# Performance work log

Hardware: AMD Instinct MI355X
Metric: run time of the kernel (lower is better)

## Reference

```python
import jax, jax.numpy as jnp
import numpy as np

N_NODES = 70000
N_EDGES = 2_000_000
IN_CH, FEAT_CH, OUT_CH = 1044, 128, 3


def _gcn_norm(src_sl, dst_sl, n_nodes, dtype):
    # PyG gcn_norm with add_self_loops=True, edge_weight=1:
    # deg over target nodes, norm = deg^-1/2[src] * deg^-1/2[dst]
    deg = jax.ops.segment_sum(jnp.ones(src_sl.shape[0], dtype=dtype), dst_sl,
                              num_segments=n_nodes)
    dinv = jnp.where(deg > 0, jax.lax.rsqrt(deg), jnp.zeros((), dtype))
    return dinv[src_sl] * dinv[dst_sl]


def _gcn_layer(x, src_sl, dst_sl, norm, W, b, n_nodes):
    h = x @ W                                  # [N, out] linear transform first
    msg = h[src_sl] * norm[:, None]            # gather + scale
    out = jax.ops.segment_sum(msg, dst_sl, num_segments=n_nodes)  # scatter-add
    return out + b


def setup_inputs() -> dict:
    key = jax.random.key(0)
    ks = jax.random.split(key, 6)
    features = jax.random.normal(ks[0], (N_NODES, IN_CH), dtype=jnp.float32)
    edges = jax.random.randint(ks[1], (2, N_EDGES), 0, N_NODES, dtype=jnp.int64)
    edges2 = jax.random.randint(ks[2], (2, N_EDGES), 0, N_NODES, dtype=jnp.int64)
    edge_features = jax.random.normal(ks[3], (N_EDGES,), dtype=jnp.float32)
    W1 = jax.random.normal(ks[4], (IN_CH, FEAT_CH), dtype=jnp.float32) * (1.0 / np.sqrt(IN_CH))
    b1 = jnp.zeros((FEAT_CH,), dtype=jnp.float32)
    W2 = jax.random.normal(ks[5], (FEAT_CH, OUT_CH), dtype=jnp.float32) * (1.0 / np.sqrt(FEAT_CH))
    b2 = jnp.zeros((OUT_CH,), dtype=jnp.float32)
    return {"features": features, "edges": edges, "edges2": edges2,
            "edge_features": edge_features, "W1": W1, "b1": b1, "W2": W2, "b2": b2}


def reference(features, edges, edges2, edge_features, W1, b1, W2, b2):
    # edge_features is discarded by the module (set to None); edges2 unused.
    n = features.shape[0]
    loop = jnp.arange(n, dtype=edges.dtype)
    src_sl = jnp.concatenate([edges[0], loop])  # self-loops appended
    dst_sl = jnp.concatenate([edges[1], loop])
    norm = _gcn_norm(src_sl, dst_sl, n, features.dtype)
    x = _gcn_layer(features, src_sl, dst_sl, norm, W1, b1, n)
    x = jax.nn.relu(x)
    # dropout is identity in eval mode (deterministic reference)
    return _gcn_layer(x, src_sl, dst_sl, norm, W2, b2, n)
```

## Files before the change

### kernel.cpp

```cpp
#include <hip/hip_runtime.h>
#include <hip/hip_bf16.h>

#define K_IN   1044
#define N_FEAT 128
#define KPAD2  1088
#define NST2   17
#define BM     96

#define NB     512
#define BWMAX  256
#define EPB    8192

typedef __attribute__((ext_vector_type(8))) short short8;
typedef __attribute__((ext_vector_type(4))) float f32x4;

__device__ __forceinline__ ushort f2bf(float f) {
  unsigned x = __float_as_uint(f);
  x += 0x7fffu + ((x >> 16) & 1u);
  return (ushort)(x >> 16);
}
__device__ __forceinline__ uint pkbf(float lo, float hi) {
  __hip_bfloat162 h = __float22bfloat162_rn(make_float2(lo, hi));
  return *reinterpret_cast<uint*>(&h);
}
__device__ __forceinline__ float bflo(uint v) { return __uint_as_float(v << 16); }
__device__ __forceinline__ float bfhi(uint v) { return __uint_as_float(v & 0xFFFF0000u); }

__device__ __forceinline__ void gld16(const void* g, void* l) {
  __builtin_amdgcn_global_load_lds(
      (const __attribute__((address_space(1))) unsigned int*)g,
      (__attribute__((address_space(3))) unsigned int*)l, 16, 0, 0);
}


__global__ __launch_bounds__(256) void convw1_hist_kernel(const float* __restrict__ W1,
                                                          ushort* __restrict__ W1T,
                                                          const int* __restrict__ dst,
                                                          int* __restrict__ bt,
                                                          int E, int bw, int convBlocks) {
  if ((int)blockIdx.x < convBlocks) {
    int idx = blockIdx.x * 256 + threadIdx.x;
    if (idx >= N_FEAT * KPAD2) return;
    int col = idx / KPAD2, k = idx - col * KPAD2;
    int kk = k & ~63;
    int jp = (k >> 3) & 7;
    int e  = k & 7;
    int jl = jp ^ (col & 7);
    int ksrc = kk + 8 * jl + e;
    W1T[idx] = (ksrc < K_IN) ? f2bf(W1[(size_t)ksrc * N_FEAT + col]) : (ushort)0;
  } else {
    __shared__ int h[NB];
    const int t = threadIdx.x;
    for (int i = t; i < NB; i += 256) h[i] = 0;
    __syncthreads();
    const int e0 = (blockIdx.x - convBlocks) * EPB;
    const int e1 = min(e0 + EPB, E);
    for (int e = e0 + t; e < e1; e += 256) atomicAdd(&h[dst[e] / bw], 1);
    __syncthreads();
    for (int i = t; i < NB; i += 256)
      if (h[i]) atomicAdd(&bt[i], h[i]);
  }
}

__global__ __launch_bounds__(256) void csr_bucket_scan_kernel(const int* __restrict__ bt,
                                                              int* __restrict__ bucket_base,
                                                              int* __restrict__ bucket_cursor) {
  __shared__ int sc[256];
  const int t = threadIdx.x;
  int v0 = bt[2 * t], v1 = bt[2 * t + 1];
  int s = v0 + v1;
  sc[t] = s;
  __syncthreads();
  for (int off = 1; off < 256; off <<= 1) {
    int x = (t >= off) ? sc[t - off] : 0;
    __syncthreads();
    sc[t] += x;
    __syncthreads();
  }
  int excl = sc[t] - s;
  bucket_base[2 * t]     = excl;
  bucket_base[2 * t + 1] = excl + v0;
  bucket_cursor[2 * t]     = excl;
  bucket_cursor[2 * t + 1] = excl + v0;
  if (t == 255) bucket_base[NB] = sc[255];
}

__global__ __launch_bounds__(256) void csr_stage_kernel(const int* __restrict__ src,
                                                        const int* __restrict__ dst,
                                                        int* __restrict__ bucket_cursor,
                                                        uint* __restrict__ staging, int E, int bw) {
  __shared__ int h[NB];
  __shared__ int cur[NB];
  const int t = threadIdx.x;
  for (int i = t; i < NB; i += 256) h[i] = 0;
  __syncthreads();
  const int e0 = blockIdx.x * EPB;
  const int e1 = min(e0 + EPB, E);
  for (int e = e0 + t; e < e1; e += 256) atomicAdd(&h[dst[e] / bw], 1);
  __syncthreads();
  for (int i = t; i < NB; i += 256)
    cur[i] = h[i] ? atomicAdd(&bucket_cursor[i], h[i]) : 0;
  __syncthreads();
  for (int e = e0 + t; e < e1; e += 256) {
    int d = dst[e];
    int b = d / bw;
    int p = atomicAdd(&cur[b], 1);
    staging[p] = ((uint)src[e] << 8) | (uint)(d - b * bw);
  }
}

__global__ __launch_bounds__(256) void csr_final_kernel(const uint* __restrict__ staging,
                                                        const int* __restrict__ bucket_base,
                                                        int* __restrict__ row_ptr,
                                                        int* __restrict__ sorted_src,
                                                        float* __restrict__ dinv,
                                                        int N, int bw, int E) {
  __shared__ int hist[BWMAX];
  __shared__ int sc[256];
  const int b = blockIdx.x;
  const int t = threadIdx.x;
  if (b == 0 && t == 0) row_ptr[N] = E;
  const int node0 = b * bw;
  const int nn = min(bw, N - node0);
  if (nn <= 0) return;
  const int base = bucket_base[b];
  const int cnt  = bucket_base[b + 1] - base;

  for (int i = t; i < BWMAX; i += 256) hist[i] = 0;
  __syncthreads();
  for (int i = t; i < cnt; i += 256)
    atomicAdd(&hist[staging[base + i] & 255u], 1);
  __syncthreads();
  int v = (t < nn) ? hist[t] : 0;
  if (t < nn) dinv[node0 + t] = rsqrtf((float)(v + 1));
  sc[t] = v;
  __syncthreads();
  for (int off = 1; off < 256; off <<= 1) {
    int x = (t >= off) ? sc[t - off] : 0;
    __syncthreads();
    sc[t] += x;
    __syncthreads();
  }
  int excl = sc[t] - v;
  if (t < nn) row_ptr[node0 + t] = base + excl;
  if (t < nn) hist[t] = excl;
  __syncthreads();
  for (int i = t; i < cnt; i += 256) {
    uint p = staging[base + i];
    int c = atomicAdd(&hist[p & 255u], 1);
    sorted_src[base + c] = (int)(p >> 8);
  }
}


__global__ __launch_bounds__(256) void gemm1_mfma_kernel(const float* __restrict__ X,
                                                         const ushort* __restrict__ W1T,
                                                         const float* __restrict__ dinv,
                                                         ushort* __restrict__ G1, int M) {
  __shared__ float  Af[2][BM * 64];
  __shared__ ushort Bsb[2][128 * 64];

  const int t = threadIdx.x;
  const int row0 = blockIdx.x * BM;
  const int w = t >> 6, l = t & 63;
  const int w24 = w * 24, w32 = w * 32;
  const int Mm1 = M - 1;

  const int wm = w >> 1, wn = w & 1;
  const int lr = l & 15, g = l >> 4;

  f32x4 acc[3][4] = {};

  auto stage = [&](int s, int buf) {
    const int kk = s * 64;
    #pragma unroll
    for (int i = 0; i < 6; i++) {
      int r  = w24 + 4 * i + (l >> 4);
      int jl = (l & 15) ^ (r & 15);
      int grow = min(row0 + r, Mm1);
      int gk   = min(kk + 4 * jl, K_IN - 4);
      gld16(X + (size_t)grow * K_IN + gk, (void*)&Af[buf][(w24 + 4 * i) * 64]);
    }
    #pragma unroll
    for (int i = 0; i < 4; i++) {
      int c = w32 + 8 * i + (l >> 3);
      gld16(W1T + (size_t)c * KPAD2 + kk + 8 * (l & 7),
            (void*)&Bsb[buf][(w32 + 8 * i) * 64]);
    }
  };

  stage(0, 0);
  __syncthreads();

  int cur = 0;
  #pragma unroll 1
  for (int s = 0; s < NST2; s++) {
    if (s + 1 < NST2) stage(s + 1, cur ^ 1);

    #pragma unroll
    for (int ss = 0; ss < 2; ss++) {
      short8 af[3], bfr[4];
      #pragma unroll
      for (int m = 0; m < 3; m++) {
        const int row = wm * 48 + m * 16 + lr;
        const float* rp = &Af[cur][row * 64];
        const int c0 = (ss * 8 + 2 * g)     ^ (row & 15);
        const int c1 = (ss * 8 + 2 * g + 1) ^ (row & 15);
        float4 a0 = *(const float4*)&rp[c0 * 4];
        float4 a1 = *(const float4*)&rp[c1 * 4];
        uint4 uu = make_uint4(pkbf(a0.x, a0.y), pkbf(a0.z, a0.w),
                              pkbf(a1.x, a1.y), pkbf(a1.z, a1.w));
        af[m] = *(short8*)&uu;
      }
      #pragma unroll
      for (int n = 0; n < 4; n++) {
        const int col = wn * 64 + n * 16 + lr;
        const int cB = (ss * 4 + g) ^ (col & 7);
        bfr[n] = *(const short8*)&Bsb[cur][col * 64 + cB * 8];
      }
      #pragma unroll
      for (int m = 0; m < 3; m++)
        #pragma unroll
        for (int n = 0; n < 4; n++)
          acc[m][n] = __builtin_amdgcn_mfma_f32_16x16x32_bf16(af[m], bfr[n], acc[m][n], 0, 0, 0);
    }

    __syncthreads();
    cur ^= 1;
  }

  const int rbase = row0 + wm * 48 + g * 4;
  const int cbase = wn * 64 + lr;
  #pragma unroll
  for (int m = 0; m < 3; m++) {
    #pragma unroll
    for (int r = 0; r < 4; r++) {
      int row = rbase + m * 16 + r;
      if (row < M) {
        float dv = dinv[row];
        #pragma unroll
        for (int n = 0; n < 4; n++)
          G1[(size_t)row * N_FEAT + cbase + n * 16] = f2bf(dv * acc[m][n][r]);
      }
    }
  }
}


__global__ __launch_bounds__(256) void agg1mm_kernel(const ushort* __restrict__ G1,
                                                     const int* __restrict__ row_ptr,
                                                     const int* __restrict__ sorted_src,
                                                     const float* __restrict__ dinv,
                                                     const float* __restrict__ b1,
                                                     const float* __restrict__ W2,
                                                     float* __restrict__ G2, int N) {
  const int w = (blockIdx.x * blockDim.x + threadIdx.x) >> 6;
  const int lane = threadIdx.x & 63;
  if (w >= N) return;
  const int beg = row_ptr[w], end = row_ptr[w + 1];
  const uint* g1u = (const uint*)G1;
  const int co = lane;

  uint vs = g1u[((size_t)w << 6) + co];
  float a0 = bflo(vs), a1 = bfhi(vs);

  int e = beg;
  for (; e + 16 <= end; e += 16) {
    int s[16];
    #pragma unroll
    for (int i = 0; i < 16; i++) s[i] = sorted_src[e + i];
    uint v[16];
    #pragma unroll
    for (int i = 0; i < 16; i++) v[i] = g1u[((size_t)s[i] << 6) + co];
    #pragma unroll
    for (int i = 0; i < 16; i++) { a0 += bflo(v[i]); a1 += bfhi(v[i]); }
  }
  for (; e + 4 <= end; e += 4) {
    int s[4];
    #pragma unroll
    for (int i = 0; i < 4; i++) s[i] = sorted_src[e + i];
    uint v[4];
    #pragma unroll
    for (int i = 0; i < 4; i++) v[i] = g1u[((size_t)s[i] << 6) + co];
    #pragma unroll
    for (int i = 0; i < 4; i++) { a0 += bflo(v[i]); a1 += bfhi(v[i]); }
  }
  for (; e < end; e++) {
    uint v = g1u[((size_t)sorted_src[e] << 6) + co];
    a0 += bflo(v); a1 += bfhi(v);
  }

  const float di = dinv[w];
  float r0 = fmaxf(fmaf(di, a0, b1[2 * co + 0]), 0.f);
  float r1 = fmaxf(fmaf(di, a1, b1[2 * co + 1]), 0.f);

  const float* wrow = W2 + 6 * co;
  float s0 = r0 * wrow[0] + r1 * wrow[3];
  float s1 = r0 * wrow[1] + r1 * wrow[4];
  float s2 = r0 * wrow[2] + r1 * wrow[5];
  #pragma unroll
  for (int off = 32; off > 0; off >>= 1) {
    s0 += __shfl_down(s0, off);
    s1 += __shfl_down(s1, off);
    s2 += __shfl_down(s2, off);
  }
  if (lane == 0) {
    *(float4*)&G2[(size_t)w * 4] = make_float4(di * s0, di * s1, di * s2, 0.f);
  }
}


__global__ __launch_bounds__(256) void agg2_kernel(const float* __restrict__ G2,
                                                   const int* __restrict__ row_ptr,
                                                   const int* __restrict__ sorted_src,
                                                   const float* __restrict__ dinv,
                                                   const float* __restrict__ b2,
                                                   float* __restrict__ out, int N) {
  int t = blockIdx.x * blockDim.x + threadIdx.x;
  int node = t >> 6, lane = t & 63;
  if (node >= N) return;
  int beg = row_ptr[node], end = row_ptr[node + 1];
  float a0 = 0.f, a1 = 0.f, a2 = 0.f;
  for (int e = beg + lane; e < end; e += 64) {
    float4 v = *(const float4*)&G2[(size_t)sorted_src[e] * 4];
    a0 += v.x; a1 += v.y; a2 += v.z;
  }
  #pragma unroll
  for (int off = 32; off > 0; off >>= 1) {
    a0 += __shfl_down(a0, off);
    a1 += __shfl_down(a1, off);
    a2 += __shfl_down(a2, off);
  }
  if (lane == 0) {
    float di = dinv[node];
    float4 self = *(const float4*)&G2[(size_t)node * 4];
    out[node * 3 + 0] = di * (a0 + self.x) + b2[0];
    out[node * 3 + 1] = di * (a1 + self.y) + b2[1];
    out[node * 3 + 2] = di * (a2 + self.z) + b2[2];
  }
}


extern "C" void kernel_launch(void* const* d_in, const int* in_sizes, int n_in,
                              void* d_out, int out_size, void* d_ws, size_t ws_size,
                              hipStream_t stream) {
  const float* features = (const float*)d_in[0];
  const int*   edges    = (const int*)d_in[1];
  const float* W1 = (const float*)d_in[4];
  const float* b1 = (const float*)d_in[5];
  const float* W2 = (const float*)d_in[6];
  const float* b2 = (const float*)d_in[7];
  float* out = (float*)d_out;

  const int N = in_sizes[0] / K_IN;
  const int E = in_sizes[1] / 2;
  const int* src = edges;
  const int* dst = edges + E;
  const int bw = (N + NB - 1) / NB;

  char* ws = (char*)d_ws;
  size_t off = 0;
  auto alloc = [&](size_t bytes) {
    void* p = ws + off;
    off += (bytes + 255) & ~(size_t)255;
    return p;
  };
  int*    bt            = (int*)   alloc((size_t)NB * sizeof(int));
  int*    bucket_base   = (int*)   alloc((size_t)(NB + 1) * sizeof(int));
  int*    bucket_cursor = (int*)   alloc((size_t)NB * sizeof(int));
  int*    row_ptr       = (int*)   alloc((size_t)(N + 1) * sizeof(int));
  float*  dinv          = (float*) alloc((size_t)N * sizeof(float));
  uint*   staging       = (uint*)  alloc((size_t)E * sizeof(uint));
  int*    sorted_src    = (int*)   alloc((size_t)E * sizeof(int));
  ushort* G1            = (ushort*)alloc((size_t)N * N_FEAT * sizeof(ushort));
  float*  G2            = (float*) alloc((size_t)N * 4 * sizeof(float));
  ushort* W1T           = (ushort*)alloc((size_t)N_FEAT * KPAD2 * sizeof(ushort));
  (void)ws_size;

  const int eblocks = (E + EPB - 1) / EPB;
  const int convBlocks = (N_FEAT * KPAD2 + 255) / 256;

  hipMemsetAsync(bt, 0, (size_t)NB * sizeof(int), stream);
  convw1_hist_kernel<<<convBlocks + eblocks, 256, 0, stream>>>(W1, W1T, dst, bt, E, bw, convBlocks);
  csr_bucket_scan_kernel<<<1, 256, 0, stream>>>(bt, bucket_base, bucket_cursor);
  csr_stage_kernel<<<eblocks, 256, 0, stream>>>(src, dst, bucket_cursor, staging, E, bw);
  csr_final_kernel<<<NB, 256, 0, stream>>>(staging, bucket_base, row_ptr, sorted_src, dinv, N, bw, E);
  gemm1_mfma_kernel<<<(N + BM - 1) / BM, 256, 0, stream>>>(features, W1T, dinv, G1, N);
  agg1mm_kernel<<<((size_t)N * 64 + 255) / 256, 256, 0, stream>>>(G1, row_ptr, sorted_src, dinv, b1, W2, G2, N);
  agg2_kernel<<<((size_t)N * 64 + 255) / 256, 256, 0, stream>>>(G2, row_ptr, sorted_src, dinv, b2, out, N);
}
```

Measured before the change: 248.7 us.

## Use per-block bucket counts with global scan; halve agg2 threads per node

The histogram kernel now writes per-block, per-bucket counts to a bucket-major matrix instead of atomically accumulating global bucket totals. A single-block scan turns that matrix into exclusive offsets and bucket bases. The stage kernel then reads its precomputed offsets directly, which removes its second histogram pass, the global atomics and the memset. Separately, agg2 assigns 32 lanes per node instead of 64 to suit the low average degree, at the cost of a serial single-block scan over about 125K entries.

```diff
diff --git a/kernel.cpp b/kernel.cpp
--- a/kernel.cpp
+++ b/kernel.cpp
@@ -36,8 +36,9 @@
 __global__ __launch_bounds__(256) void convw1_hist_kernel(const float* __restrict__ W1,
                                                           ushort* __restrict__ W1T,
                                                           const int* __restrict__ dst,
-                                                          int* __restrict__ bt,
-                                                          int E, int bw, int convBlocks) {
+                                                          int* __restrict__ pbc,
+                                                          int E, int bw, int convBlocks,
+                                                          int eblocks) {
   if ((int)blockIdx.x < convBlocks) {
     int idx = blockIdx.x * 256 + threadIdx.x;
     if (idx >= N_FEAT * KPAD2) return;
@@ -51,56 +52,57 @@
   } else {
     __shared__ int h[NB];
     const int t = threadIdx.x;
+    const int blk = blockIdx.x - convBlocks;
     for (int i = t; i < NB; i += 256) h[i] = 0;
     __syncthreads();
-    const int e0 = (blockIdx.x - convBlocks) * EPB;
+    const int e0 = blk * EPB;
     const int e1 = min(e0 + EPB, E);
     for (int e = e0 + t; e < e1; e += 256) atomicAdd(&h[dst[e] / bw], 1);
     __syncthreads();
-    for (int i = t; i < NB; i += 256)
-      if (h[i]) atomicAdd(&bt[i], h[i]);
-  }
-}
-
-__global__ __launch_bounds__(256) void csr_bucket_scan_kernel(const int* __restrict__ bt,
-                                                              int* __restrict__ bucket_base,
-                                                              int* __restrict__ bucket_cursor) {
-  __shared__ int sc[256];
+    for (int i = t; i < NB; i += 256) pbc[i * eblocks + blk] = h[i];
+  }
+}
+
+__global__ __launch_bounds__(256) void csr_scan2_kernel(int* __restrict__ pbc,
+                                                        int* __restrict__ bucket_base,
+                                                        int eblocks, int total, int E) {
+  __shared__ int sums[256];
   const int t = threadIdx.x;
-  int v0 = bt[2 * t], v1 = bt[2 * t + 1];
-  int s = v0 + v1;
-  sc[t] = s;
+  const int chunk = (total + 255) / 256;
+  const int beg = t * chunk;
+  const int end = min(beg + chunk, total);
+  int s = 0;
+  for (int i = beg; i < end; i++) s += pbc[i];
+  sums[t] = s;
   __syncthreads();
   for (int off = 1; off < 256; off <<= 1) {
-    int x = (t >= off) ? sc[t - off] : 0;
-    __syncthreads();
-    sc[t] += x;
-    __syncthreads();
-  }
-  int excl = sc[t] - s;
-  bucket_base[2 * t]     = excl;
-  bucket_base[2 * t + 1] = excl + v0;
-  bucket_cursor[2 * t]     = excl;
-  bucket_cursor[2 * t + 1] = excl + v0;
-  if (t == 255) bucket_base[NB] = sc[255];
+    int x = (t >= off) ? sums[t - off] : 0;
+    __syncthreads();
+    sums[t] += x;
+    __syncthreads();
+  }
+  int run = sums[t] - s;
+  for (int i = beg; i < end; i++) {
+    int v = pbc[i];
+    pbc[i] = run;
+    if (i % eblocks == 0) bucket_base[i / eblocks] = run;
+    run += v;
+  }
+  if (t == 255) bucket_base[NB] = E;
 }
 
 __global__ __launch_bounds__(256) void csr_stage_kernel(const int* __restrict__ src,
                                                         const int* __restrict__ dst,
-                                                        int* __restrict__ bucket_cursor,
-                                                        uint* __restrict__ staging, int E, int bw) {
-  __shared__ int h[NB];
+                                                        const int* __restrict__ pbc,
+                                                        uint* __restrict__ staging, int E, int bw,
+                                                        int eblocks) {
   __shared__ int cur[NB];
   const int t = threadIdx.x;
-  for (int i = t; i < NB; i += 256) h[i] = 0;
-  __syncthreads();
-  const int e0 = blockIdx.x * EPB;
+  const int blk = blockIdx.x;
+  for (int i = t; i < NB; i += 256) cur[i] = pbc[i * eblocks + blk];
+  __syncthreads();
+  const int e0 = blk * EPB;
   const int e1 = min(e0 + EPB, E);
-  for (int e = e0 + t; e < e1; e += 256) atomicAdd(&h[dst[e] / bw], 1);
-  __syncthreads();
-  for (int i = t; i < NB; i += 256)
-    cur[i] = h[i] ? atomicAdd(&bucket_cursor[i], h[i]) : 0;
-  __syncthreads();
   for (int e = e0 + t; e < e1; e += 256) {
     int d = dst[e];
     int b = d / bw;
@@ -317,19 +319,19 @@
                                                    const float* __restrict__ b2,
                                                    float* __restrict__ out, int N) {
   int t = blockIdx.x * blockDim.x + threadIdx.x;
-  int node = t >> 6, lane = t & 63;
+  int node = t >> 5, lane = t & 31;
   if (node >= N) return;
   int beg = row_ptr[node], end = row_ptr[node + 1];
   float a0 = 0.f, a1 = 0.f, a2 = 0.f;
-  for (int e = beg + lane; e < end; e += 64) {
+  for (int e = beg + lane; e < end; e += 32) {
     float4 v = *(const float4*)&G2[(size_t)sorted_src[e] * 4];
     a0 += v.x; a1 += v.y; a2 += v.z;
   }
   #pragma unroll
-  for (int off = 32; off > 0; off >>= 1) {
-    a0 += __shfl_down(a0, off);
-    a1 += __shfl_down(a1, off);
-    a2 += __shfl_down(a2, off);
+  for (int off = 16; off > 0; off >>= 1) {
+    a0 += __shfl_down(a0, off, 32);
+    a1 += __shfl_down(a1, off, 32);
+    a2 += __shfl_down(a2, off, 32);
   }
   if (lane == 0) {
     float di = dinv[node];
@@ -365,9 +367,10 @@
     off += (bytes + 255) & ~(size_t)255;
     return p;
   };
-  int*    bt            = (int*)   alloc((size_t)NB * sizeof(int));
+  const int eblocks = (E + EPB - 1) / EPB;
+
+  int*    pbc           = (int*)   alloc((size_t)NB * eblocks * sizeof(int));
   int*    bucket_base   = (int*)   alloc((size_t)(NB + 1) * sizeof(int));
-  int*    bucket_cursor = (int*)   alloc((size_t)NB * sizeof(int));
   int*    row_ptr       = (int*)   alloc((size_t)(N + 1) * sizeof(int));
   float*  dinv          = (float*) alloc((size_t)N * sizeof(float));
   uint*   staging       = (uint*)  alloc((size_t)E * sizeof(uint));
@@ -377,15 +380,13 @@
   ushort* W1T           = (ushort*)alloc((size_t)N_FEAT * KPAD2 * sizeof(ushort));
   (void)ws_size;
 
-  const int eblocks = (E + EPB - 1) / EPB;
   const int convBlocks = (N_FEAT * KPAD2 + 255) / 256;
 
-  hipMemsetAsync(bt, 0, (size_t)NB * sizeof(int), stream);
-  convw1_hist_kernel<<<convBlocks + eblocks, 256, 0, stream>>>(W1, W1T, dst, bt, E, bw, convBlocks);
-  csr_bucket_scan_kernel<<<1, 256, 0, stream>>>(bt, bucket_base, bucket_cursor);
-  csr_stage_kernel<<<eblocks, 256, 0, stream>>>(src, dst, bucket_cursor, staging, E, bw);
+  convw1_hist_kernel<<<convBlocks + eblocks, 256, 0, stream>>>(W1, W1T, dst, pbc, E, bw, convBlocks, eblocks);
+  csr_scan2_kernel<<<1, 256, 0, stream>>>(pbc, bucket_base, eblocks, NB * eblocks, E);
+  csr_stage_kernel<<<eblocks, 256, 0, stream>>>(src, dst, pbc, staging, E, bw, eblocks);
   csr_final_kernel<<<NB, 256, 0, stream>>>(staging, bucket_base, row_ptr, sorted_src, dinv, N, bw, E);
   gemm1_mfma_kernel<<<(N + BM - 1) / BM, 256, 0, stream>>>(features, W1T, dinv, G1, N);
   agg1mm_kernel<<<((size_t)N * 64 + 255) / 256, 256, 0, stream>>>(G1, row_ptr, sorted_src, dinv, b1, W2, G2, N);
-  agg2_kernel<<<((size_t)N * 64 + 255) / 256, 256, 0, stream>>>(G2, row_ptr, sorted_src, dinv, b2, out, N);
-}
+  agg2_kernel<<<((size_t)N * 32 + 255) / 256, 256, 0, stream>>>(G2, row_ptr, sorted_src, dinv, b2, out, N);
+}
```

After: 433.5 us. 74.3% more time.
